# Performance work log

Hardware: AMD Instinct MI355X
Metric: run time of the kernel (lower is better)

Reference implementation:

```python
import jax, jax.numpy as jnp
import numpy as np

N_NODES = 50000
N_EDGES = 400000
DIMS = [512, 512, 512, 512]  # input + 3 hidden
NUM_CLASSES = 40


def setup_inputs() -> dict:
    key = jax.random.key(0)
    ks = jax.random.split(key, 16)
    feat = jax.random.normal(ks[0], (N_NODES, DIMS[0]), dtype=jnp.float32)
    src = jax.random.randint(ks[1], (N_EDGES,), 0, N_NODES, dtype=jnp.int32)
    dst = jax.random.randint(ks[2], (N_EDGES,), 0, N_NODES, dtype=jnp.int32)
    params = {}
    for i in range(3):
        fan_in = DIMS[i]
        s = 1.0 / np.sqrt(fan_in)
        params[f"W{i}"] = jax.random.uniform(ks[3 + 2 * i], (DIMS[i], DIMS[i + 1]), jnp.float32, -s, s)
        params[f"b{i}"] = jax.random.uniform(ks[4 + 2 * i], (DIMS[i + 1],), jnp.float32, -s, s)
    s = 1.0 / np.sqrt(DIMS[-1])
    params["Wc"] = jax.random.uniform(ks[10], (DIMS[-1], NUM_CLASSES), jnp.float32, -s, s)
    params["bc"] = jax.random.uniform(ks[11], (NUM_CLASSES,), jnp.float32, -s, s)
    return {"feat": feat, "src": src, "dst": dst, **params}


def _gin_layer(h, src, dst, W, b):
    # DGL GINConv, aggregator='sum', eps=0: rst = (1+eps)*h + sum_{j in N(i)} h_j
    agg = jax.ops.segment_sum(h[src], dst, num_segments=N_NODES)  # [N, D]
    return jax.nn.relu((h + agg) @ W + b)  # apply_func Linear, then relu (dropout p=0)


def reference(feat, src, dst, W0, b0, W1, b1, W2, b2, Wc, bc):
    h = _gin_layer(feat, src, dst, W0, b0)
    h = _gin_layer(h, src, dst, W1, b1)
    h = _gin_layer(h, src, dst, W2, b2)
    return h @ Wc + bc  # [N, num_classes]
```

## Files before the change

### kernel.cpp

```cpp
#include <hip/hip_runtime.h>

#define N_NODES 50000
#define N_EDGES 400000
#define D 512
#define NCLS 40
#define SCAN_BLOCKS ((N_NODES + 255) / 256)

typedef __attribute__((ext_vector_type(8))) __bf16 bf16x8;
typedef __attribute__((ext_vector_type(4))) float f32x4;
typedef __attribute__((ext_vector_type(4))) float float4v;
typedef __attribute__((ext_vector_type(8))) unsigned short ushort8v;
typedef __attribute__((ext_vector_type(4))) unsigned short ushort4v;

#define AS1 __attribute__((address_space(1)))
#define AS3 __attribute__((address_space(3)))

__device__ __forceinline__ float bf2f(unsigned short u) {
  union { unsigned int i; float f; } v; v.i = ((unsigned int)u) << 16; return v.f;
}
__device__ __forceinline__ unsigned short f2bf(float f) {
  union { float f; unsigned int i; } v; v.f = f;
  unsigned int u = v.i;
  u += 0x7fffu + ((u >> 16) & 1u);
  return (unsigned short)(u >> 16);
}

__global__ void hist_kernel(const int* __restrict__ dst, int* __restrict__ counts) {
  int e = blockIdx.x * blockDim.x + threadIdx.x;
  if (e < N_EDGES) atomicAdd(&counts[dst[e]], 1);
}

__global__ __launch_bounds__(256) void scan_local_kernel(const int* __restrict__ counts,
    int* __restrict__ incl, int* __restrict__ bsum) {
  __shared__ int s[256];
  int i = blockIdx.x * 256 + threadIdx.x;
  int v = (i < N_NODES) ? counts[i] : 0;
  s[threadIdx.x] = v;
  __syncthreads();
#pragma unroll
  for (int o = 1; o < 256; o <<= 1) {
    int t = (threadIdx.x >= o) ? s[threadIdx.x - o] : 0;
    __syncthreads();
    s[threadIdx.x] += t;
    __syncthreads();
  }
  if (i < N_NODES) incl[i] = s[threadIdx.x];
  if (threadIdx.x == 255) bsum[blockIdx.x] = s[255];
}

__global__ __launch_bounds__(256) void scan_bsum_kernel(int* __restrict__ bsum) {
  __shared__ int s[256];
  int v = (threadIdx.x < SCAN_BLOCKS) ? bsum[threadIdx.x] : 0;
  s[threadIdx.x] = v;
  __syncthreads();
#pragma unroll
  for (int o = 1; o < 256; o <<= 1) {
    int t = (threadIdx.x >= o) ? s[threadIdx.x - o] : 0;
    __syncthreads();
    s[threadIdx.x] += t;
    __syncthreads();
  }
  if (threadIdx.x < SCAN_BLOCKS) bsum[threadIdx.x] = s[threadIdx.x] - v;
}

__global__ __launch_bounds__(256) void scan_finish_kernel(const int* __restrict__ counts,
    const int* __restrict__ bsum, int* __restrict__ row_ptr, int* __restrict__ cursor) {
  int i = blockIdx.x * 256 + threadIdx.x;
  if (i < N_NODES) {
    int inc = cursor[i] + bsum[blockIdx.x];
    row_ptr[i + 1] = inc;
    cursor[i] = inc - counts[i];
    if (i == 0) row_ptr[0] = 0;
  }
}

__global__ void fill_kernel(const int* __restrict__ src, const int* __restrict__ dst,
                            int* __restrict__ cursor, int* __restrict__ esrc) {
  int e = blockIdx.x * blockDim.x + threadIdx.x;
  if (e < N_EDGES) {
    int pos = atomicAdd(&cursor[dst[e]], 1);
    esrc[pos] = src[e];
  }
}

__global__ void cvt_feat_kernel(const float* __restrict__ feat, unsigned short* __restrict__ hb) {
  size_t i = (size_t)(blockIdx.x * blockDim.x + threadIdx.x) * 4;
  if (i < (size_t)N_NODES * D) {
    float4v v = *(const float4v*)&feat[i];
    ushort4v o;
    o[0] = f2bf(v[0]); o[1] = f2bf(v[1]); o[2] = f2bf(v[2]); o[3] = f2bf(v[3]);
    *(ushort4v*)&hb[i] = o;
  }
}

__global__ void cvt_w3_kernel(const float* __restrict__ W0, const float* __restrict__ W1,
                              const float* __restrict__ W2, unsigned short* __restrict__ Wt) {
  int i = blockIdx.x * blockDim.x + threadIdx.x;
  int l = i >> 18;
  int r = i & 262143;
  int n = r >> 9, k = r & 511;
  const float* W = (l == 0) ? W0 : ((l == 1) ? W1 : W2);
  Wt[i] = f2bf(W[k * D + n]);
}

__global__ void cvt_wc_kernel(const float* __restrict__ Wc, unsigned short* __restrict__ Wct) {
  int i = blockIdx.x * blockDim.x + threadIdx.x;
  if (i < 48 * D) {
    int n = i >> 9, k = i & 511;
    Wct[i] = (n < NCLS) ? f2bf(Wc[k * NCLS + n]) : (unsigned short)0;
  }
}

__global__ __launch_bounds__(256) void agg_kernel(const unsigned short* __restrict__ hb,
    const int* __restrict__ row_ptr, const int* __restrict__ esrc,
    unsigned short* __restrict__ zb) {
  int w = threadIdx.x >> 6, lane = threadIdx.x & 63;
  int node = blockIdx.x * 4 + w;
  int col = lane * 8;
  const unsigned short* hcol = hb + col;
  float acc[8];
  ushort8v v = *(const ushort8v*)&hcol[(size_t)node * D];
#pragma unroll
  for (int t = 0; t < 8; ++t) acc[t] = bf2f(v[t]);
  int s = row_ptr[node], e = row_ptr[node + 1];
  int j = s;
  for (; j + 4 <= e; j += 4) {
    int i0 = esrc[j + 0], i1 = esrc[j + 1], i2 = esrc[j + 2], i3 = esrc[j + 3];
    ushort8v v0 = *(const ushort8v*)&hcol[(size_t)i0 * D];
    ushort8v v1 = *(const ushort8v*)&hcol[(size_t)i1 * D];
    ushort8v v2 = *(const ushort8v*)&hcol[(size_t)i2 * D];
    ushort8v v3 = *(const ushort8v*)&hcol[(size_t)i3 * D];
#pragma unroll
    for (int t = 0; t < 8; ++t) acc[t] += bf2f(v0[t]);
#pragma unroll
    for (int t = 0; t < 8; ++t) acc[t] += bf2f(v1[t]);
#pragma unroll
    for (int t = 0; t < 8; ++t) acc[t] += bf2f(v2[t]);
#pragma unroll
    for (int t = 0; t < 8; ++t) acc[t] += bf2f(v3[t]);
  }
  for (; j < e; ++j) {
    int sn = esrc[j];
    ushort8v nv = *(const ushort8v*)&hcol[(size_t)sn * D];
#pragma unroll
    for (int t = 0; t < 8; ++t) acc[t] += bf2f(nv[t]);
  }
  ushort8v o;
#pragma unroll
  for (int t = 0; t < 8; ++t) o[t] = f2bf(acc[t]);
  *(ushort8v*)&zb[(size_t)node * D + col] = o;
}

__global__ __launch_bounds__(256) void gemm_kernel(
    const unsigned short* __restrict__ Z, const unsigned short* __restrict__ Wt,
    const float* __restrict__ bias, unsigned short* __restrict__ Hout, int M) {
  __shared__ unsigned short smem[128 * 132];
  unsigned short* As = smem;
  unsigned short* Bs = smem + 8192;
  const int n0 = blockIdx.x * 128;
  const int m0 = blockIdx.y * 128;
  const int tid = threadIdx.x;
  const int lane = tid & 63;
  const int w = tid >> 6;
  const int wm = (w & 1) * 64;
  const int wn = (w >> 1) * 64;
  const int quad = lane >> 4;
  const int r16 = lane & 15;
  const int srow = lane >> 3;
  const int sslot = lane & 7;

  f32x4 acc[4][4];
#pragma unroll
  for (int i = 0; i < 4; ++i)
#pragma unroll
    for (int j = 0; j < 4; ++j)
      acc[i][j] = (f32x4){0.f, 0.f, 0.f, 0.f};

  for (int kt = 0; kt < 8; ++kt) {
    __syncthreads();
    const int kbase = kt * 64;
#pragma unroll
    for (int c = 0; c < 4; ++c) {
      int r0 = w * 32 + c * 8;
      int row = r0 + srow;
      int gk = kbase + (sslot ^ (row & 7)) * 8;
      int gm = m0 + row; if (gm > M - 1) gm = M - 1;
      __builtin_amdgcn_global_load_lds(
          (AS1 void*)(void*)(Z + (size_t)gm * D + gk),
          (AS3 void*)(As + r0 * 64), 16, 0, 0);
      int gn = n0 + row;
      __builtin_amdgcn_global_load_lds(
          (AS1 void*)(void*)(Wt + (size_t)gn * D + gk),
          (AS3 void*)(Bs + r0 * 64), 16, 0, 0);
    }
    __syncthreads();

#pragma unroll
    for (int half = 0; half < 2; ++half) {
      bf16x8 a[4], b[4];
#pragma unroll
      for (int i = 0; i < 4; ++i) {
        int ra = wm + i * 16 + r16;
        a[i] = *(const bf16x8*)&As[ra * 64 + (((half << 2) + quad) ^ (ra & 7)) * 8];
        int rb = wn + i * 16 + r16;
        b[i] = *(const bf16x8*)&Bs[rb * 64 + (((half << 2) + quad) ^ (rb & 7)) * 8];
      }
#pragma unroll
      for (int i = 0; i < 4; ++i)
#pragma unroll
        for (int j = 0; j < 4; ++j)
          acc[i][j] = __builtin_amdgcn_mfma_f32_16x16x32_bf16(a[i], b[j], acc[i][j], 0, 0, 0);
    }
  }

  __syncthreads();
  unsigned short* Cs = smem;
#pragma unroll
  for (int j = 0; j < 4; ++j) {
    float bv = bias[n0 + wn + j * 16 + r16];
#pragma unroll
    for (int i = 0; i < 4; ++i) {
      int crow = wm + i * 16 + quad * 4;
      int ccol = wn + j * 16 + r16;
#pragma unroll
      for (int r = 0; r < 4; ++r) {
        float vv = acc[i][j][r] + bv;
        vv = vv > 0.f ? vv : 0.f;
        Cs[(crow + r) * 132 + ccol] = f2bf(vv);
      }
    }
  }
  __syncthreads();
#pragma unroll
  for (int it = 0; it < 8; ++it) {
    int row = w * 32 + it * 4 + (lane >> 4);
    int colofs = (lane & 15) * 8;
    int gm = m0 + row;
    if (gm < M) {
      ushort8v vv = *(const ushort8v*)&Cs[row * 132 + colofs];
      *(ushort8v*)&Hout[(size_t)gm * D + n0 + colofs] = vv;
    }
  }
}

__global__ __launch_bounds__(256) void cls_kernel(const unsigned short* __restrict__ hb,
    const unsigned short* __restrict__ Wct, const float* __restrict__ bc,
    float* __restrict__ out) {
  int w = threadIdx.x >> 6, lane = threadIdx.x & 63;
  int quad = lane >> 4, r16 = lane & 15;
  int nb = blockIdx.x * 64 + w * 16;
  int arow = nb + r16; if (arow > N_NODES - 1) arow = N_NODES - 1;
  f32x4 acc[3];
#pragma unroll
  for (int j = 0; j < 3; ++j) acc[j] = (f32x4){0.f, 0.f, 0.f, 0.f};
#pragma unroll 4
  for (int kt = 0; kt < 16; ++kt) {
    int kk = kt * 32 + quad * 8;
    bf16x8 a = *(const bf16x8*)&hb[(size_t)arow * D + kk];
#pragma unroll
    for (int j = 0; j < 3; ++j) {
      bf16x8 b = *(const bf16x8*)&Wct[(size_t)(j * 16 + r16) * D + kk];
      acc[j] = __builtin_amdgcn_mfma_f32_16x16x32_bf16(a, b, acc[j], 0, 0, 0);
    }
  }
#pragma unroll
  for (int j = 0; j < 3; ++j) {
    int gn = j * 16 + r16;
    if (gn < NCLS) {
      float bv = bc[gn];
#pragma unroll
      for (int r = 0; r < 4; ++r) {
        int gm = nb + quad * 4 + r;
        if (gm < N_NODES) out[(size_t)gm * NCLS + gn] = acc[j][r] + bv;
      }
    }
  }
}

extern "C" void kernel_launch(void* const* d_in, const int* in_sizes, int n_in,
                              void* d_out, int out_size, void* d_ws, size_t ws_size,
                              hipStream_t stream) {
  const float* feat = (const float*)d_in[0];
  const int* src = (const int*)d_in[1];
  const int* dst = (const int*)d_in[2];
  const float* W0 = (const float*)d_in[3];
  const float* b0 = (const float*)d_in[4];
  const float* W1 = (const float*)d_in[5];
  const float* b1 = (const float*)d_in[6];
  const float* W2 = (const float*)d_in[7];
  const float* b2 = (const float*)d_in[8];
  const float* Wc = (const float*)d_in[9];
  const float* bc = (const float*)d_in[10];
  float* out = (float*)d_out;

  char* ws = (char*)d_ws;
  size_t off = 0;
  auto alloc = [&](size_t bytes) {
    char* p = ws + off;
    off += (bytes + 255) & ~(size_t)255;
    return p;
  };
  unsigned short* hb = (unsigned short*)alloc((size_t)N_NODES * D * 2);
  unsigned short* zb = (unsigned short*)alloc((size_t)N_NODES * D * 2);
  unsigned short* Wt = (unsigned short*)alloc((size_t)3 * D * D * 2);
  unsigned short* Wct = (unsigned short*)alloc((size_t)48 * D * 2);
  int* row_ptr = (int*)alloc((size_t)(N_NODES + 1) * 4);
  int* counts  = (int*)alloc((size_t)N_NODES * 4);
  int* cursor  = (int*)alloc((size_t)N_NODES * 4);
  int* esrc    = (int*)alloc((size_t)N_EDGES * 4);
  int* bsum    = (int*)alloc((size_t)256 * 4);

  hipMemsetAsync(counts, 0, (size_t)N_NODES * 4, stream);
  hist_kernel<<<(N_EDGES + 255) / 256, 256, 0, stream>>>(dst, counts);
  scan_local_kernel<<<SCAN_BLOCKS, 256, 0, stream>>>(counts, cursor, bsum);
  scan_bsum_kernel<<<1, 256, 0, stream>>>(bsum);
  scan_finish_kernel<<<SCAN_BLOCKS, 256, 0, stream>>>(counts, bsum, row_ptr, cursor);
  fill_kernel<<<(N_EDGES + 255) / 256, 256, 0, stream>>>(src, dst, cursor, esrc);

  cvt_feat_kernel<<<(N_NODES * D / 4 + 255) / 256, 256, 0, stream>>>(feat, hb);
  cvt_w3_kernel<<<3 * 262144 / 256, 256, 0, stream>>>(W0, W1, W2, Wt);
  cvt_wc_kernel<<<(48 * D + 255) / 256, 256, 0, stream>>>(Wc, Wct);

  dim3 ggrid(4, (N_NODES + 127) / 128);
  const float* bs[3] = {b0, b1, b2};
  for (int l = 0; l < 3; ++l) {
    agg_kernel<<<N_NODES / 4, 256, 0, stream>>>(hb, row_ptr, esrc, zb);
    gemm_kernel<<<ggrid, 256, 0, stream>>>(zb, Wt + (size_t)l * D * D, bs[l], hb, N_NODES);
  }
  cls_kernel<<<(N_NODES + 63) / 64, 256, 0, stream>>>(hb, Wct, bc, out);
}
```

Before: 627.6 us.

## Restructure GEMM to 64-row full-width tiles with A resident in LDS and B from global

The GEMM now gives each block 64 rows across all 512 output columns. The whole 64x512 A tile is loaded into LDS once, and each wave reads its weight fragments directly from global memory (L2-cached) instead of staging them through LDS. This removes the four-way re-read of Z across column blocks and the per-k-tile LDS syncs, at the cost of more register accumulators (32 f32x4), uncoalesced global B loads in the inner loop, and a 65KB LDS footprint that limits occupancy. The two weight-conversion kernels are also merged into a single launch.

```diff
diff --git a/kernel.cpp b/kernel.cpp
--- a/kernel.cpp
+++ b/kernel.cpp
@@ -5,6 +5,7 @@
 #define D 512
 #define NCLS 40
 #define SCAN_BLOCKS ((N_NODES + 255) / 256)
+#define CSTRIDE 520
 
 typedef __attribute__((ext_vector_type(8))) __bf16 bf16x8;
 typedef __attribute__((ext_vector_type(4))) float f32x4;
@@ -93,21 +94,22 @@
   }
 }
 
-__global__ void cvt_w3_kernel(const float* __restrict__ W0, const float* __restrict__ W1,
-                              const float* __restrict__ W2, unsigned short* __restrict__ Wt) {
+__global__ void cvt_w_all_kernel(const float* __restrict__ W0, const float* __restrict__ W1,
+                                 const float* __restrict__ W2, const float* __restrict__ Wc,
+                                 unsigned short* __restrict__ Wt, unsigned short* __restrict__ Wct) {
   int i = blockIdx.x * blockDim.x + threadIdx.x;
-  int l = i >> 18;
-  int r = i & 262143;
-  int n = r >> 9, k = r & 511;
-  const float* W = (l == 0) ? W0 : ((l == 1) ? W1 : W2);
-  Wt[i] = f2bf(W[k * D + n]);
-}
-
-__global__ void cvt_wc_kernel(const float* __restrict__ Wc, unsigned short* __restrict__ Wct) {
-  int i = blockIdx.x * blockDim.x + threadIdx.x;
-  if (i < 48 * D) {
-    int n = i >> 9, k = i & 511;
-    Wct[i] = (n < NCLS) ? f2bf(Wc[k * NCLS + n]) : (unsigned short)0;
+  if (i < 3 * D * D) {
+    int l = i >> 18;
+    int r = i & (D * D - 1);
+    int n = r >> 9, k = r & 511;
+    const float* W = (l == 0) ? W0 : ((l == 1) ? W1 : W2);
+    Wt[i] = f2bf(W[k * D + n]);
+  } else {
+    int r = i - 3 * D * D;
+    if (r < 48 * D) {
+      int n = r >> 9, k = r & 511;
+      Wct[r] = (n < NCLS) ? f2bf(Wc[k * NCLS + n]) : (unsigned short)0;
+    }
   }
 }
 
@@ -154,91 +156,78 @@
 __global__ __launch_bounds__(256) void gemm_kernel(
     const unsigned short* __restrict__ Z, const unsigned short* __restrict__ Wt,
     const float* __restrict__ bias, unsigned short* __restrict__ Hout, int M) {
-  __shared__ unsigned short smem[128 * 132];
+  __shared__ unsigned short smem[64 * CSTRIDE];
   unsigned short* As = smem;
-  unsigned short* Bs = smem + 8192;
-  const int n0 = blockIdx.x * 128;
-  const int m0 = blockIdx.y * 128;
+  const int m0 = blockIdx.x * 64;
   const int tid = threadIdx.x;
   const int lane = tid & 63;
   const int w = tid >> 6;
-  const int wm = (w & 1) * 64;
-  const int wn = (w >> 1) * 64;
-  const int quad = lane >> 4;
-  const int r16 = lane & 15;
-  const int srow = lane >> 3;
-  const int sslot = lane & 7;
-
-  f32x4 acc[4][4];
+  const int quad = lane >> 4, r16 = lane & 15;
+  const int wn = w * 128;
+
+#pragma unroll
+  for (int i = 0; i < 16; ++i) {
+    int row = w * 16 + i;
+    int gm = m0 + row; if (gm > M - 1) gm = M - 1;
+    int gchunk = lane ^ (row & 7);
+    __builtin_amdgcn_global_load_lds(
+        (AS1 void*)(void*)(Z + (size_t)gm * D + gchunk * 8),
+        (AS3 void*)(As + row * 512), 16, 0, 0);
+  }
+  __syncthreads();
+
+  f32x4 acc[4][8];
 #pragma unroll
   for (int i = 0; i < 4; ++i)
 #pragma unroll
-    for (int j = 0; j < 4; ++j)
-      acc[i][j] = (f32x4){0.f, 0.f, 0.f, 0.f};
-
-  for (int kt = 0; kt < 8; ++kt) {
-    __syncthreads();
-    const int kbase = kt * 64;
-#pragma unroll
-    for (int c = 0; c < 4; ++c) {
-      int r0 = w * 32 + c * 8;
-      int row = r0 + srow;
-      int gk = kbase + (sslot ^ (row & 7)) * 8;
-      int gm = m0 + row; if (gm > M - 1) gm = M - 1;
-      __builtin_amdgcn_global_load_lds(
-          (AS1 void*)(void*)(Z + (size_t)gm * D + gk),
-          (AS3 void*)(As + r0 * 64), 16, 0, 0);
-      int gn = n0 + row;
-      __builtin_amdgcn_global_load_lds(
-          (AS1 void*)(void*)(Wt + (size_t)gn * D + gk),
-          (AS3 void*)(Bs + r0 * 64), 16, 0, 0);
-    }
-    __syncthreads();
-
-#pragma unroll
-    for (int half = 0; half < 2; ++half) {
-      bf16x8 a[4], b[4];
-#pragma unroll
-      for (int i = 0; i < 4; ++i) {
-        int ra = wm + i * 16 + r16;
-        a[i] = *(const bf16x8*)&As[ra * 64 + (((half << 2) + quad) ^ (ra & 7)) * 8];
-        int rb = wn + i * 16 + r16;
-        b[i] = *(const bf16x8*)&Bs[rb * 64 + (((half << 2) + quad) ^ (rb & 7)) * 8];
-      }
+    for (int j = 0; j < 8; ++j) acc[i][j] = (f32x4){0.f, 0.f, 0.f, 0.f};
+
+#pragma unroll 4
+  for (int kt = 0; kt < 16; ++kt) {
+    bf16x8 a[4];
+#pragma unroll
+    for (int i = 0; i < 4; ++i) {
+      int row = i * 16 + r16;
+      int slot = (kt * 4 + quad) ^ (row & 7);
+      a[i] = *(const bf16x8*)&As[row * 512 + slot * 8];
+    }
+#pragma unroll
+    for (int j = 0; j < 8; ++j) {
+      bf16x8 b = *(const bf16x8*)&Wt[(size_t)(wn + j * 16 + r16) * D + kt * 32 + quad * 8];
 #pragma unroll
       for (int i = 0; i < 4; ++i)
-#pragma unroll
-        for (int j = 0; j < 4; ++j)
-          acc[i][j] = __builtin_amdgcn_mfma_f32_16x16x32_bf16(a[i], b[j], acc[i][j], 0, 0, 0);
+        acc[i][j] = __builtin_amdgcn_mfma_f32_16x16x32_bf16(a[i], b, acc[i][j], 0, 0, 0);
     }
   }
 
   __syncthreads();
   unsigned short* Cs = smem;
 #pragma unroll
-  for (int j = 0; j < 4; ++j) {
-    float bv = bias[n0 + wn + j * 16 + r16];
+  for (int j = 0; j < 8; ++j) {
+    float bv = bias[wn + j * 16 + r16];
 #pragma unroll
     for (int i = 0; i < 4; ++i) {
-      int crow = wm + i * 16 + quad * 4;
-      int ccol = wn + j * 16 + r16;
 #pragma unroll
       for (int r = 0; r < 4; ++r) {
+        int m = i * 16 + quad * 4 + r;
         float vv = acc[i][j][r] + bv;
         vv = vv > 0.f ? vv : 0.f;
-        Cs[(crow + r) * 132 + ccol] = f2bf(vv);
+        Cs[m * CSTRIDE + wn + j * 16 + r16] = f2bf(vv);
       }
     }
   }
   __syncthreads();
 #pragma unroll
-  for (int it = 0; it < 8; ++it) {
-    int row = w * 32 + it * 4 + (lane >> 4);
-    int colofs = (lane & 15) * 8;
+  for (int it = 0; it < 4; ++it) {
+    int row = w * 16 + it * 4 + (lane >> 4);
     int gm = m0 + row;
-    if (gm < M) {
-      ushort8v vv = *(const ushort8v*)&Cs[row * 132 + colofs];
-      *(ushort8v*)&Hout[(size_t)gm * D + n0 + colofs] = vv;
+#pragma unroll
+    for (int cc = 0; cc < 4; ++cc) {
+      int colofs = cc * 128 + (lane & 15) * 8;
+      if (gm < M) {
+        ushort8v vv = *(const ushort8v*)&Cs[row * CSTRIDE + colofs];
+        *(ushort8v*)&Hout[(size_t)gm * D + colofs] = vv;
+      }
     }
   }
 }
@@ -318,14 +307,12 @@
   fill_kernel<<<(N_EDGES + 255) / 256, 256, 0, stream>>>(src, dst, cursor, esrc);
 
   cvt_feat_kernel<<<(N_NODES * D / 4 + 255) / 256, 256, 0, stream>>>(feat, hb);
-  cvt_w3_kernel<<<3 * 262144 / 256, 256, 0, stream>>>(W0, W1, W2, Wt);
-  cvt_wc_kernel<<<(48 * D + 255) / 256, 256, 0, stream>>>(Wc, Wct);
-
-  dim3 ggrid(4, (N_NODES + 127) / 128);
+  cvt_w_all_kernel<<<(3 * D * D + 48 * D + 255) / 256, 256, 0, stream>>>(W0, W1, W2, Wc, Wt, Wct);
+
   const float* bs[3] = {b0, b1, b2};
   for (int l = 0; l < 3; ++l) {
     agg_kernel<<<N_NODES / 4, 256, 0, stream>>>(hb, row_ptr, esrc, zb);
-    gemm_kernel<<<ggrid, 256, 0, stream>>>(zb, Wt + (size_t)l * D * D, bs[l], hb, N_NODES);
+    gemm_kernel<<<(N_NODES + 63) / 64, 256, 0, stream>>>(zb, Wt + (size_t)l * D * D, bs[l], hb, N_NODES);
   }
   cls_kernel<<<(N_NODES + 63) / 64, 256, 0, stream>>>(hb, Wct, bc, out);
 }
```

Measured after the change: 881.9 us. +40.5%, slower.
